# Kernel tuning notes

Measured on AMD Instinct MI355X. Metric: run time of the kernel, lower is better.

The kernel has to match this reference:

```python
import jax, jax.numpy as jnp
import numpy as np

QW_MAX = 127  # 2**(8-1) - 1


def setup_inputs() -> dict:
    key = jax.random.key(0)
    k1, k2, k3, k4, k5 = jax.random.split(key, 5)
    B, Din, H, Dout = 4096, 1024, 4096, 1024
    x = jax.random.normal(k1, (B, Din), dtype=jnp.float32)
    # float master weights (already transposed, as in quantify_weights: weight.T)
    w1f = jax.random.normal(k2, (Din, H), dtype=jnp.float32) * 0.02
    b1f = jax.random.normal(k3, (H,), dtype=jnp.float32) * 0.02
    w2f = jax.random.normal(k4, (H, Dout), dtype=jnp.float32) * 0.02
    b2f = jax.random.normal(k5, (Dout,), dtype=jnp.float32) * 0.02
    return {"x": x, "w1f": w1f, "b1f": b1f, "w2f": w2f, "b2f": b2f}


def _quantify_pair(w, b):
    # joint max-abs scale over weight and bias (matches quantify(x, x2))
    max_v = jnp.maximum(jnp.max(jnp.abs(w)), jnp.max(jnp.abs(b)))
    scale = max_v / QW_MAX
    wq = jnp.round(w / scale).astype(jnp.int8)
    bq = jnp.round(b / scale).astype(jnp.int8)
    return wq, bq, scale


def _dot_product(q_a, q_b, scale_a, scale_b, target_scale):
    # int8 GEMM with int32 accumulation, then requantize to int16
    y0 = q_a.astype(jnp.int32) @ q_b.astype(jnp.int32)  # [M, N] int32
    scale = scale_a * scale_b / target_scale
    return jnp.round(y0 * scale).astype(jnp.int16)


def reference(x, w1f, b1f, w2f, b2f):
    # weight quantization (done once at init in torch, inlined here)
    w1, b1, s1 = _quantify_pair(w1f, b1f)
    w2, b2, s2 = _quantify_pair(w2f, b2f)
    # dynamic activation quantization
    x_scale = jnp.max(jnp.abs(x)) / QW_MAX
    x_q = jnp.round(x / x_scale).astype(jnp.int8)
    # layer 1: target_scale = s1, so effective multiplier is x_scale
    o1 = _dot_product(x_q, w1, x_scale, s1, s1) + b1.astype(jnp.int16)
    # layer 2: note torch passes scale_1 (not x_scale) here — faithful to source
    o2 = _dot_product(jnp.maximum(o1, 0), w2, s1, s2, s2) + b2.astype(jnp.int16)
    # dequantize
    return o2.astype(jnp.float32) * s2
```

## Files before the change

kernel.cpp:

```cpp
#include <hip/hip_runtime.h>
#include <stdint.h>

typedef int   i32x4 __attribute__((ext_vector_type(4)));
typedef float f32x4 __attribute__((ext_vector_type(4)));

#define WS_PART    0
#define WS_XQ      32768
#define WS_W1QT    (WS_XQ   + 4096*1024)
#define WS_W2QT    (WS_W1QT + 4096*1024)
#define WS_PS      (WS_W2QT + 4096*1024)
#define WS_PH      (WS_PS   + 4096*4096)

__device__ __forceinline__ void async16(const void* g, void* l) {
  __builtin_amdgcn_global_load_lds(
      (const __attribute__((address_space(1))) unsigned*)g,
      (__attribute__((address_space(3))) unsigned*)l, 16, 0, 0);
}

__device__ __forceinline__ float block_absmax(const float* __restrict__ p0, int n0,
                                              const float* __restrict__ p1, int n1,
                                              float* red, float* slot) {
  int tid = threadIdx.x, nt = blockDim.x;
  float m = 0.f;
  for (int i = tid; i < n0; i += nt) m = fmaxf(m, fabsf(p0[i]));
  if (p1) for (int i = tid; i < n1; i += nt) m = fmaxf(m, fabsf(p1[i]));
  for (int off = 32; off; off >>= 1) m = fmaxf(m, __shfl_down(m, off));
  if ((tid & 63) == 0) red[tid >> 6] = m;
  __syncthreads();
  if (tid == 0) {
    int nw = nt >> 6;
    float M = red[0];
    for (int w = 1; w < nw; w++) M = fmaxf(M, red[w]);
    *slot = M;
  }
  __syncthreads();
  return *slot;
}

__global__ void k_absmax3(const float* __restrict__ x, const float* __restrict__ w1,
                          const float* __restrict__ w2, float* __restrict__ part) {
  int seg = blockIdx.x >> 9;
  int b = blockIdx.x & 511;
  const float* p = (seg == 0) ? x : (seg == 1) ? w1 : w2;
  int i = b * 256 + threadIdx.x;
  float m = 0.f;
  #pragma unroll
  for (int it = 0; it < 8; it++) {
    f32x4 v = ((const f32x4*)p)[i + it * 131072];
    m = fmaxf(m, fmaxf(fmaxf(fabsf(v.x), fabsf(v.y)), fmaxf(fabsf(v.z), fabsf(v.w))));
  }
  for (int off = 32; off; off >>= 1) m = fmaxf(m, __shfl_down(m, off));
  __shared__ float red[4];
  if ((threadIdx.x & 63) == 0) red[threadIdx.x >> 6] = m;
  __syncthreads();
  if (threadIdx.x == 0)
    part[blockIdx.x] = fmaxf(fmaxf(red[0], red[1]), fmaxf(red[2], red[3]));
}

__device__ __forceinline__ void quantT_body(const float* __restrict__ w, float s,
                                            i32x4* __restrict__ out, int C, int tkbits,
                                            int b) {
  int L = b * 256 + threadIdx.x;
  int h_in = L & 127;
  int kb = (L >> 7) & 3;
  int tk = (L >> 9) & ((1 << tkbits) - 1);
  int hblk = L >> (9 + tkbits);
  int h = hblk * 128 + h_in;
  int k0 = (tk * 4 + kb) * 16;
  int wd[4];
  #pragma unroll
  for (int d = 0; d < 4; d++) {
    unsigned acc = 0;
    #pragma unroll
    for (int j = 0; j < 4; j++) {
      float v = w[(size_t)(k0 + d * 4 + j) * C + h];
      int q = (int)rintf(v / s) & 255;
      acc |= (unsigned)q << (8 * j);
    }
    wd[d] = (int)acc;
  }
  i32x4 o; o.x = wd[0]; o.y = wd[1]; o.z = wd[2]; o.w = wd[3];
  out[L] = o;
}

__global__ void k_prep(const float* __restrict__ x, const float* __restrict__ w1f,
                       const float* __restrict__ w2f, const float* __restrict__ b1f,
                       const float* __restrict__ b2f, const float* __restrict__ part,
                       i32x4* __restrict__ xq, i32x4* __restrict__ w1qt,
                       i32x4* __restrict__ w2qt) {
  __shared__ float red[4];
  __shared__ float slot;
  int seg = blockIdx.x >> 10;
  int b = blockIdx.x & 1023;
  if (seg == 0) {
    float s = block_absmax(part, 512, nullptr, 0, red, &slot) / 127.0f;
    int L = b * 256 + threadIdx.x;
    int m_in = L & 127, kb = (L >> 7) & 3, tk = (L >> 9) & 15, mblk = L >> 13;
    int m = mblk * 128 + m_in;
    int k0 = (tk * 4 + kb) * 16;
    const f32x4* px = (const f32x4*)(x + m * 1024 + k0);
    int wd[4];
    #pragma unroll
    for (int d = 0; d < 4; d++) {
      f32x4 v = px[d];
      int b0 = (int)rintf(v.x / s) & 255;
      int b1 = (int)rintf(v.y / s) & 255;
      int b2 = (int)rintf(v.z / s) & 255;
      int b3 = (int)rintf(v.w / s) & 255;
      wd[d] = b0 | (b1 << 8) | (b2 << 16) | (b3 << 24);
    }
    i32x4 o; o.x = wd[0]; o.y = wd[1]; o.z = wd[2]; o.w = wd[3];
    xq[L] = o;
  } else if (seg == 1) {
    float s = block_absmax(part + 512, 512, b1f, 4096, red, &slot) / 127.0f;
    quantT_body(w1f, s, w1qt, 4096, 4, b);
  } else {
    float s = block_absmax(part + 1024, 512, b2f, 1024, red, &slot) / 127.0f;
    quantT_body(w2f, s, w2qt, 1024, 6, b);
  }
}

__launch_bounds__(256)
__global__ void k_gemm1(const i32x4* __restrict__ Aq, const i32x4* __restrict__ Bq,
                        const float* __restrict__ part, const float* __restrict__ b1f,
                        unsigned* __restrict__ plane_s, unsigned* __restrict__ plane_h) {
  __shared__ float red[4];
  __shared__ float slot;
  __shared__ int b1s[128];
  int tid = threadIdx.x;
  int bb = blockIdx.x;
  int hb = blockIdx.y;
  int lane = tid & 63, wid = tid >> 6;
  int wm = wid & 1, wn = wid >> 1;
  int g = lane >> 4, l15 = lane & 15;

  const i32x4* gA = Aq + (size_t)hb * 16 * 512;
  const i32x4* gB = Bq + (size_t)bb * 16 * 512;
  int aoff = g * 128 + wm * 64 + l15;
  int boff = g * 128 + wn * 64 + l15;

  float sx  = block_absmax(part, 512, nullptr, 0, red, &slot) / 127.0f;
  float s1v = block_absmax(part + 512, 512, b1f, 4096, red, &slot) / 127.0f;
  float mult1 = sx * s1v / s1v;
  for (int i = tid; i < 128; i += 256)
    b1s[i] = (int)rintf(b1f[hb * 128 + i] / s1v);
  __syncthreads();

  i32x4 acc[4][4];
  #pragma unroll
  for (int r = 0; r < 4; r++)
    #pragma unroll
    for (int c = 0; c < 4; c++) acc[r][c] = (i32x4)(0);

  i32x4 af[4], bf[4];
  #pragma unroll
  for (int r = 0; r < 4; r++) af[r] = gA[aoff + r * 16];
  #pragma unroll
  for (int c = 0; c < 4; c++) bf[c] = gB[boff + c * 16];

  for (int t = 0; t < 15; ++t) {
    i32x4 an[4], bn[4];
    const i32x4* ga = gA + (t + 1) * 512;
    const i32x4* gb = gB + (t + 1) * 512;
    #pragma unroll
    for (int r = 0; r < 4; r++) an[r] = ga[aoff + r * 16];
    #pragma unroll
    for (int c = 0; c < 4; c++) bn[c] = gb[boff + c * 16];
    #pragma unroll
    for (int r = 0; r < 4; r++)
      #pragma unroll
      for (int c = 0; c < 4; c++)
        acc[r][c] = __builtin_amdgcn_mfma_i32_16x16x64_i8(af[r], bf[c], acc[r][c], 0, 0, 0);
    #pragma unroll
    for (int r = 0; r < 4; r++) { af[r] = an[r]; bf[r] = bn[r]; }
  }
  #pragma unroll
  for (int r = 0; r < 4; r++)
    #pragma unroll
    for (int c = 0; c < 4; c++)
      acc[r][c] = __builtin_amdgcn_mfma_i32_16x16x64_i8(af[r], bf[c], acc[r][c], 0, 0, 0);

  int t2base = hb * 2 + wm;
  #pragma unroll
  for (int r = 0; r < 4; r++) {
    int hloc = wm * 64 + r * 16 + 4 * g;
    int bq0 = b1s[hloc], bq1 = b1s[hloc + 1], bq2 = b1s[hloc + 2], bq3 = b1s[hloc + 3];
    #pragma unroll
    for (int c = 0; c < 4; c++) {
      unsigned lo = 0, hi = 0;
      #pragma unroll
      for (int q = 0; q < 4; q++) {
        int y0 = acc[r][c][q];
        int bqv = (q == 0) ? bq0 : (q == 1) ? bq1 : (q == 2) ? bq2 : bq3;
        int o = (short)((int)rintf((float)y0 * mult1) + bqv);
        int a = o > 0 ? o : 0;
        int s8 = (int)(signed char)(a & 0xFF);
        int h8 = (a >> 8) + (s8 < 0 ? 1 : 0);
        lo |= (unsigned)(s8 & 0xFF) << (8 * q);
        hi |= (unsigned)(h8 & 0xFF) << (8 * q);
      }
      int m_in = wn * 64 + c * 16 + l15;
      unsigned idx = (((unsigned)(bb * 64 + t2base) * 512u + (unsigned)(r * 128 + m_in)) << 2) + g;
      plane_s[idx] = lo;
      plane_h[idx] = hi;
    }
  }
}

__launch_bounds__(512, 4)
__global__ void k_gemm2(const i32x4* __restrict__ Ps, const i32x4* __restrict__ Ph,
                        const i32x4* __restrict__ Bq, const float* __restrict__ part,
                        const float* __restrict__ b1f, const float* __restrict__ b2f,
                        float* __restrict__ out) {
  __shared__ i32x4 st[2048];
  __shared__ float red[8];
  __shared__ float slot;

  int tid = threadIdx.x;
  int L = blockIdx.x;
  int mb = ((L & 7) << 3) | ((L >> 3) & 7);
  int nb = L >> 6;
  int mblk = mb >> 1, half = mb & 1;
  int wid = tid >> 6, lane = tid & 63;
  int kh = wid >> 2, w2 = wid & 3;
  int wm = w2 & 1, wn = w2 >> 1;
  int g = lane >> 4, l15 = lane & 15;
  int t256 = tid & 255;
  int sbase = kh * 1024;
  int a_idx = (t256 >> 6) * 128 + half * 64 + (t256 & 63);
  int b_idx = g * 128 + wn * 64 + l15;

  {
    int t = kh * 32;
    const i32x4* pS = Ps + ((size_t)(mblk * 64 + t) << 9);
    const i32x4* pH = Ph + ((size_t)(mblk * 64 + t) << 9);
    async16(pS + a_idx, &st[sbase + t256]);
    async16(pH + a_idx, &st[sbase + 256 + t256]);
  }
  i32x4 bf[4];
  {
    const i32x4* pB = Bq + ((size_t)(nb * 64 + kh * 32) << 9);
    #pragma unroll
    for (int c = 0; c < 4; c++) bf[c] = pB[b_idx + c * 16];
  }

  float s1v = block_absmax(part + 512, 512, b1f, 4096, red, &slot) / 127.0f;
  float s2v = block_absmax(part + 1024, 512, b2f, 1024, red, &slot) / 127.0f;
  float mult2 = s1v * s2v / s2v;
  int bq[4];
  #pragma unroll
  for (int c = 0; c < 4; c++)
    bq[c] = (int)rintf(b2f[nb * 128 + wn * 64 + c * 16 + l15] / s2v);

  i32x4 accS[2][4], accH[2][4];
  #pragma unroll
  for (int r = 0; r < 2; r++)
    #pragma unroll
    for (int c = 0; c < 4; c++) { accS[r][c] = (i32x4)(0); accH[r][c] = (i32x4)(0); }

  for (int tt = 0; tt < 32; ++tt) {
    int cur = tt & 1;
    __syncthreads();
    if (tt + 1 < 32) {
      int t = kh * 32 + tt + 1;
      const i32x4* pS = Ps + ((size_t)(mblk * 64 + t) << 9);
      const i32x4* pH = Ph + ((size_t)(mblk * 64 + t) << 9);
      int R1 = sbase + (cur ^ 1) * 512;
      async16(pS + a_idx, &st[R1 + t256]);
      async16(pH + a_idx, &st[R1 + 256 + t256]);
    }
    int R = sbase + cur * 512;
    i32x4 aS[2], aH[2];
    #pragma unroll
    for (int r = 0; r < 2; r++) {
      aS[r] = st[R + g * 64 + wm * 32 + r * 16 + l15];
      aH[r] = st[R + 256 + g * 64 + wm * 32 + r * 16 + l15];
    }
    #pragma unroll
    for (int r = 0; r < 2; r++)
      #pragma unroll
      for (int c = 0; c < 4; c++) {
        accS[r][c] = __builtin_amdgcn_mfma_i32_16x16x64_i8(aS[r], bf[c], accS[r][c], 0, 0, 0);
        accH[r][c] = __builtin_amdgcn_mfma_i32_16x16x64_i8(aH[r], bf[c], accH[r][c], 0, 0, 0);
      }
    if (tt + 1 < 32) {
      const i32x4* pB = Bq + ((size_t)(nb * 64 + kh * 32 + tt + 1) << 9);
      #pragma unroll
      for (int c = 0; c < 4; c++) bf[c] = pB[b_idx + c * 16];
    }
  }

  int y0p[2][4][4];
  #pragma unroll
  for (int r = 0; r < 2; r++)
    #pragma unroll
    for (int c = 0; c < 4; c++)
      #pragma unroll
      for (int q = 0; q < 4; q++)
        y0p[r][c][q] = accS[r][c][q] + accH[r][c][q] * 256;

  __syncthreads();
  int* mg = (int*)st;
  if (kh == 1) {
    #pragma unroll
    for (int r = 0; r < 2; r++)
      #pragma unroll
      for (int c = 0; c < 4; c++)
        #pragma unroll
        for (int q = 0; q < 4; q++)
          mg[((r * 4 + c) * 4 + q) * 256 + t256] = y0p[r][c][q];
  }
  __syncthreads();
  if (kh == 0) {
    #pragma unroll
    for (int r = 0; r < 2; r++) {
      int m0 = mb * 64 + wm * 32 + r * 16 + 4 * g;
      #pragma unroll
      for (int c = 0; c < 4; c++) {
        int n = nb * 128 + wn * 64 + c * 16 + l15;
        #pragma unroll
        for (int q = 0; q < 4; q++) {
          int y0 = y0p[r][c][q] + mg[((r * 4 + c) * 4 + q) * 256 + t256];
          int o = (short)((int)rintf((float)y0 * mult2) + bq[c]);
          out[(size_t)(m0 + q) * 1024 + n] = (float)o * s2v;
        }
      }
    }
  }
}

extern "C" void kernel_launch(void* const* d_in, const int* in_sizes, int n_in,
                              void* d_out, int out_size, void* d_ws, size_t ws_size,
                              hipStream_t stream) {
  const float* x   = (const float*)d_in[0];
  const float* w1f = (const float*)d_in[1];
  const float* b1f = (const float*)d_in[2];
  const float* w2f = (const float*)d_in[3];
  const float* b2f = (const float*)d_in[4];
  float* out = (float*)d_out;

  char* ws = (char*)d_ws;
  float*  part    = (float*)(ws + WS_PART);
  i32x4*  xq      = (i32x4*)(ws + WS_XQ);
  i32x4*  w1qt    = (i32x4*)(ws + WS_W1QT);
  i32x4*  w2qt    = (i32x4*)(ws + WS_W2QT);
  unsigned* ps    = (unsigned*)(ws + WS_PS);
  unsigned* ph    = (unsigned*)(ws + WS_PH);

  k_absmax3<<<1536, 256, 0, stream>>>(x, w1f, w2f, part);
  k_prep<<<3072, 256, 0, stream>>>(x, w1f, w2f, b1f, b2f, part, xq, w1qt, w2qt);
  k_gemm1<<<dim3(32, 32), 256, 0, stream>>>(w1qt, xq, part, b1f, ps, ph);
  k_gemm2<<<512, 512, 0, stream>>>((const i32x4*)ps, (const i32x4*)ph, w2qt,
                                   part, b1f, b2f, out);
}
```

Before: 194.7 us.

## Precompute scales in prep and split gemm1 blocks into single-wave blocks

k_prep now writes the three quantization scales to workspace, so k_gemm1 reads them directly instead of running two block-wide absmax reductions per block. k_gemm1 is relaunched with one 64-thread wave per block (grid z=4) rather than four waves sharing a block, which removes the shared-memory bias table and the barrier. Bias quantization is done per lane from global memory. Since the waves already loaded their operands straight from global memory, no data sharing is lost, but scheduling granularity and the redundant bias loads change.

```diff
diff --git a/kernel.cpp b/kernel.cpp
--- a/kernel.cpp
+++ b/kernel.cpp
@@ -86,6 +86,7 @@
 __global__ void k_prep(const float* __restrict__ x, const float* __restrict__ w1f,
                        const float* __restrict__ w2f, const float* __restrict__ b1f,
                        const float* __restrict__ b2f, const float* __restrict__ part,
+                       float* __restrict__ scales,
                        i32x4* __restrict__ xq, i32x4* __restrict__ w1qt,
                        i32x4* __restrict__ w2qt) {
   __shared__ float red[4];
@@ -94,6 +95,7 @@
   int b = blockIdx.x & 1023;
   if (seg == 0) {
     float s = block_absmax(part, 512, nullptr, 0, red, &slot) / 127.0f;
+    if (b == 0 && threadIdx.x == 0) scales[0] = s;
     int L = b * 256 + threadIdx.x;
     int m_in = L & 127, kb = (L >> 7) & 3, tk = (L >> 9) & 15, mblk = L >> 13;
     int m = mblk * 128 + m_in;
@@ -113,24 +115,23 @@
     xq[L] = o;
   } else if (seg == 1) {
     float s = block_absmax(part + 512, 512, b1f, 4096, red, &slot) / 127.0f;
+    if (b == 0 && threadIdx.x == 0) scales[1] = s;
     quantT_body(w1f, s, w1qt, 4096, 4, b);
   } else {
     float s = block_absmax(part + 1024, 512, b2f, 1024, red, &slot) / 127.0f;
+    if (b == 0 && threadIdx.x == 0) scales[2] = s;
     quantT_body(w2f, s, w2qt, 1024, 6, b);
   }
 }
 
-__launch_bounds__(256)
+__launch_bounds__(64)
 __global__ void k_gemm1(const i32x4* __restrict__ Aq, const i32x4* __restrict__ Bq,
-                        const float* __restrict__ part, const float* __restrict__ b1f,
+                        const float* __restrict__ scales, const float* __restrict__ b1f,
                         unsigned* __restrict__ plane_s, unsigned* __restrict__ plane_h) {
-  __shared__ float red[4];
-  __shared__ float slot;
-  __shared__ int b1s[128];
-  int tid = threadIdx.x;
+  int lane = threadIdx.x;
   int bb = blockIdx.x;
   int hb = blockIdx.y;
-  int lane = tid & 63, wid = tid >> 6;
+  int wid = blockIdx.z;
   int wm = wid & 1, wn = wid >> 1;
   int g = lane >> 4, l15 = lane & 15;
 
@@ -139,12 +140,9 @@
   int aoff = g * 128 + wm * 64 + l15;
   int boff = g * 128 + wn * 64 + l15;
 
-  float sx  = block_absmax(part, 512, nullptr, 0, red, &slot) / 127.0f;
-  float s1v = block_absmax(part + 512, 512, b1f, 4096, red, &slot) / 127.0f;
+  float sx  = scales[0];
+  float s1v = scales[1];
   float mult1 = sx * s1v / s1v;
-  for (int i = tid; i < 128; i += 256)
-    b1s[i] = (int)rintf(b1f[hb * 128 + i] / s1v);
-  __syncthreads();
 
   i32x4 acc[4][4];
   #pragma unroll
@@ -184,7 +182,10 @@
   #pragma unroll
   for (int r = 0; r < 4; r++) {
     int hloc = wm * 64 + r * 16 + 4 * g;
-    int bq0 = b1s[hloc], bq1 = b1s[hloc + 1], bq2 = b1s[hloc + 2], bq3 = b1s[hloc + 3];
+    int bq0 = (int)rintf(b1f[hb * 128 + hloc + 0] / s1v);
+    int bq1 = (int)rintf(b1f[hb * 128 + hloc + 1] / s1v);
+    int bq2 = (int)rintf(b1f[hb * 128 + hloc + 2] / s1v);
+    int bq3 = (int)rintf(b1f[hb * 128 + hloc + 3] / s1v);
     #pragma unroll
     for (int c = 0; c < 4; c++) {
       unsigned lo = 0, hi = 0;
@@ -341,6 +342,7 @@
 
   char* ws = (char*)d_ws;
   float*  part    = (float*)(ws + WS_PART);
+  float*  scales  = part + 1536;
   i32x4*  xq      = (i32x4*)(ws + WS_XQ);
   i32x4*  w1qt    = (i32x4*)(ws + WS_W1QT);
   i32x4*  w2qt    = (i32x4*)(ws + WS_W2QT);
@@ -348,8 +350,8 @@
   unsigned* ph    = (unsigned*)(ws + WS_PH);
 
   k_absmax3<<<1536, 256, 0, stream>>>(x, w1f, w2f, part);
-  k_prep<<<3072, 256, 0, stream>>>(x, w1f, w2f, b1f, b2f, part, xq, w1qt, w2qt);
-  k_gemm1<<<dim3(32, 32), 256, 0, stream>>>(w1qt, xq, part, b1f, ps, ph);
+  k_prep<<<3072, 256, 0, stream>>>(x, w1f, w2f, b1f, b2f, part, scales, xq, w1qt, w2qt);
+  k_gemm1<<<dim3(32, 32, 4), 64, 0, stream>>>(w1qt, xq, scales, b1f, ps, ph);
   k_gemm2<<<512, 512, 0, stream>>>((const i32x4*)ps, (const i32x4*)ph, w2qt,
                                    part, b1f, b2f, out);
 }
```

Measured after the change: 183.9 us. -5.5%, faster.
